# Optimization experiments

Hardware: AMD Instinct MI355X
Metric: run time of the kernel (lower is better)

## Reference

```python
import jax, jax.numpy as jnp
import numpy as np

B, L, D, KSIZE = 16, 2048, 128, 8  # batch, seq_len, d_model (=input=hidden), window size


def setup_inputs() -> dict:
    key = jax.random.key(0)
    ks = jax.random.split(key, 5)
    s = 1.0 / np.sqrt(D)  # PyTorch RNN init range
    return {
        "x": jax.random.normal(ks[0], (B, L, D), jnp.float32),
        "W_ih": jax.random.uniform(ks[1], (3 * D, D), jnp.float32, -s, s),
        "W_hh": jax.random.uniform(ks[2], (3 * D, D), jnp.float32, -s, s),
        "b_ih": jax.random.uniform(ks[3], (3 * D,), jnp.float32, -s, s),
        "b_hh": jax.random.uniform(ks[4], (3 * D,), jnp.float32, -s, s),
    }


def _local_gru(x, W_ih, W_hh, b_ih, b_hh, ksize):
    # x: [B, L, D]. Equivalent to get_K (left zero-pad + sliding windows of
    # length ksize) followed by a GRU over each window, keeping the last
    # hidden state. Instead of materializing [B*L, ksize, D] windows, we scan
    # over the ksize window positions: at step t, every window reads the
    # shifted sequence x_pad[:, t:t+L, :].
    Bb, Ll, Dd = x.shape
    H = W_hh.shape[1]
    pad = jnp.zeros((Bb, ksize - 1, Dd), x.dtype)
    xp = jnp.concatenate([pad, x], axis=1)  # [B, L+k-1, D]
    xs = jnp.stack([xp[:, t:t + Ll, :] for t in range(ksize)], axis=0)  # [k, B, L, D]

    Wir, Wiz, Win = jnp.split(W_ih, 3, axis=0)
    Whr, Whz, Whn = jnp.split(W_hh, 3, axis=0)
    bir, biz, bin_ = jnp.split(b_ih, 3)
    bhr, bhz, bhn = jnp.split(b_hh, 3)

    def step(h, xt):  # h, xt: [B, L, H/D]
        r = jax.nn.sigmoid(xt @ Wir.T + bir + h @ Whr.T + bhr)
        z = jax.nn.sigmoid(xt @ Wiz.T + biz + h @ Whz.T + bhz)
        n = jnp.tanh(xt @ Win.T + bin_ + r * (h @ Whn.T + bhn))
        h = (1.0 - z) * n + z * h
        return h, None

    h0 = jnp.zeros((Bb, Ll, H), x.dtype)
    h_last, _ = jax.lax.scan(step, h0, xs)
    return h_last  # [B, L, H]: last hidden state of each length-ksize window


def reference(x, W_ih, W_hh, b_ih, b_hh):
    return _local_gru(x, W_ih, W_hh, b_ih, b_hh, KSIZE)
```

## Files before the change

### kernel.cpp

```cpp
#include <hip/hip_runtime.h>
#include <hip/hip_bf16.h>

#define DEV __device__ __forceinline__

typedef __attribute__((ext_vector_type(8))) short bf16x8;
typedef __attribute__((ext_vector_type(4))) float f32x4;

constexpr int Bq = 16, Lq = 2048, Dq = 128;
constexpr int RZ = 2 * Dq;
constexpr float L2E = 1.4426950408889634f;

DEV float exp2f_hw(float x) { return __builtin_amdgcn_exp2f(x); }

DEV unsigned short f2bf(float f) {
    union { __hip_bfloat16 h; unsigned short u; } v;
    v.h = __float2bfloat16(f);
    return v.u;
}
DEV float bfu_lo(int u) { return __uint_as_float((unsigned)u << 16); }
DEV float bfu_hi(int u) { return __uint_as_float((unsigned)u & 0xffff0000u); }

DEV float sigm2(float y) { return __builtin_amdgcn_rcpf(1.f + exp2f_hw(-y)); }
DEV float tanh2(float y) {
    float e = exp2f_hw(y);
    return fmaf(-2.f, __builtin_amdgcn_rcpf(e + 1.f), 1.f);
}

DEV bf16x8 pack8s(float4 a, float4 b, float s) {
    bf16x8 r;
    r[0] = (short)f2bf(a.x * s); r[1] = (short)f2bf(a.y * s);
    r[2] = (short)f2bf(a.z * s); r[3] = (short)f2bf(a.w * s);
    r[4] = (short)f2bf(b.x * s); r[5] = (short)f2bf(b.y * s);
    r[6] = (short)f2bf(b.z * s); r[7] = (short)f2bf(b.w * s);
    return r;
}
DEV int2 packbf4(float a, float b, float c, float d) {
    int2 r;
    r.x = (int)(((unsigned)f2bf(b) << 16) | (unsigned)f2bf(a));
    r.y = (int)(((unsigned)f2bf(d) << 16) | (unsigned)f2bf(c));
    return r;
}

__global__ __launch_bounds__(512, 2) void k_proj(
    const float* __restrict__ x, const float* __restrict__ W_ih,
    const float* __restrict__ b_ih, const float* __restrict__ b_hh,
    unsigned short* __restrict__ XpT)
{
    __shared__ __attribute__((aligned(16))) unsigned char lds[96 * 64 * 8];

    const int tid = threadIdx.x;
    const int lane = tid & 63, w = tid >> 6;
    const int l15 = lane & 15, l4 = lane >> 4;
    const int r0 = blockIdx.x * 64;

#pragma unroll
    for (int it = 0; it < 4; ++it) {
        int c = it * 512 + tid;
        int byte = c << 4;
        int row = byte >> 9;
        int wb = byte & 511;
        float4 v = *(const float4*)((const char*)(x + (size_t)r0 * Dq) + byte);
        int dst = row * 256 + ((wb >> 1) ^ ((row & 7) << 4));
        *(int2*)(lds + dst) = packbf4(v.x, v.y, v.z, v.w);
    }

    bf16x8 afr[3][4];
#pragma unroll
    for (int mt = 0; mt < 3; ++mt)
#pragma unroll
        for (int kc = 0; kc < 4; ++kc) {
            int row = 48 * w + 16 * mt + l15;
            int k0 = 32 * kc + 8 * l4;
            const float* p = W_ih + row * Dq + k0;
            afr[mt][kc] = pack8s(*(const float4*)p, *(const float4*)(p + 4), 1.f);
        }
    float fs[3], bias[3][4];
#pragma unroll
    for (int mt = 0; mt < 3; ++mt) {
        int rbase = 48 * w + 16 * mt + 4 * l4;
        fs[mt] = (rbase < RZ) ? L2E : 2.f * L2E;
#pragma unroll
        for (int r = 0; r < 4; ++r) {
            int row = rbase + r;
            float bv = b_ih[row] + (row < RZ ? b_hh[row] : 0.f);
            bias[mt][r] = bv * fs[mt];
        }
    }
    __syncthreads();

    f32x4 acc[3][4];
#pragma unroll
    for (int mt = 0; mt < 3; ++mt)
#pragma unroll
        for (int nt = 0; nt < 4; ++nt) {
            acc[mt][nt][0] = 0.f; acc[mt][nt][1] = 0.f;
            acc[mt][nt][2] = 0.f; acc[mt][nt][3] = 0.f;
        }

#pragma unroll
    for (int kc = 0; kc < 4; ++kc) {
        bf16x8 bfr[4];
#pragma unroll
        for (int nt = 0; nt < 4; ++nt) {
            int row = 16 * nt + l15;
            int off = row * 256 + ((64 * kc + 16 * l4) ^ ((row & 7) << 4));
            bfr[nt] = *(const bf16x8*)(lds + off);
        }
#pragma unroll
        for (int nt = 0; nt < 4; ++nt)
#pragma unroll
            for (int mt = 0; mt < 3; ++mt)
                acc[mt][nt] = __builtin_amdgcn_mfma_f32_16x16x32_bf16(
                    afr[mt][kc], bfr[nt], acc[mt][nt], 0, 0, 0);
    }

    __syncthreads();

#pragma unroll
    for (int mt = 0; mt < 3; ++mt)
#pragma unroll
        for (int nt = 0; nt < 4; ++nt) {
            int r = 16 * nt + l15;
            int g4 = 12 * w + 4 * mt + l4;
            int2 pk = packbf4(fmaf(acc[mt][nt][0], fs[mt], bias[mt][0]),
                              fmaf(acc[mt][nt][1], fs[mt], bias[mt][1]),
                              fmaf(acc[mt][nt][2], fs[mt], bias[mt][2]),
                              fmaf(acc[mt][nt][3], fs[mt], bias[mt][3]));
            *(int2*)(lds + (((g4 << 6) + r) << 3)) = pk;
        }
    __syncthreads();

    {
        const int lr0 = r0 & 2047;
        const int bb = r0 >> 11;
#pragma unroll
        for (int it = 0; it < 6; ++it) {
            int idx = it * 512 + tid;
            int g4 = idx >> 5, off = idx & 31;
            size_t d = (((size_t)(bb * 96 + g4) << 11) + lr0) >> 1;
            ((int4*)XpT)[d + off] = ((const int4*)lds)[idx];
        }
    }
}

__global__ __launch_bounds__(512, 2) void k_rnn(
    const int2* __restrict__ Xp2, const float* __restrict__ W_hh,
    const float* __restrict__ b_ih, const float* __restrict__ b_hh,
    float* __restrict__ out)
{
    __shared__ __attribute__((aligned(16))) unsigned char hls[2 * 32 * 256];

    const int tid = threadIdx.x;
    const int lane = tid & 63, w = tid >> 6;
    const int l15 = lane & 15, l4 = lane >> 4;
    const int b = blockIdx.x >> 6;
    const int l0 = (blockIdx.x & 63) << 5;

    bf16x8 afr[3][4];
#pragma unroll
    for (int g = 0; g < 3; ++g) {
        float fg = (g < 2) ? L2E : 2.f * L2E;
#pragma unroll
        for (int kc = 0; kc < 4; ++kc) {
            int row = 128 * g + 16 * w + l15;
            int k0 = 32 * kc + 8 * l4;
            const float* p = W_hh + row * Dq + k0;
            afr[g][kc] = pack8s(*(const float4*)p, *(const float4*)(p + 4), fg);
        }
    }
    const int u0 = 16 * w + 4 * l4;
    const float4 bir = *(const float4*)(b_ih + u0);
    const float4 bhr = *(const float4*)(b_hh + u0);
    const float4 biz = *(const float4*)(b_ih + Dq + u0);
    const float4 bhz = *(const float4*)(b_hh + Dq + u0);
    const float4 bin_ = *(const float4*)(b_ih + RZ + u0);
    const float4 bhn = *(const float4*)(b_hh + RZ + u0);
    f32x4 bhn4;
    bhn4[0] = bhn.x * (2.f * L2E); bhn4[1] = bhn.y * (2.f * L2E);
    bhn4[2] = bhn.z * (2.f * L2E); bhn4[3] = bhn.w * (2.f * L2E);
    const int2 pbr = packbf4((bir.x + bhr.x) * L2E, (bir.y + bhr.y) * L2E,
                             (bir.z + bhr.z) * L2E, (bir.w + bhr.w) * L2E);
    const int2 pbz = packbf4((biz.x + bhz.x) * L2E, (biz.y + bhz.y) * L2E,
                             (biz.z + bhz.z) * L2E, (biz.w + bhz.w) * L2E);
    const int2 pbn = packbf4(bin_.x * (2.f * L2E), bin_.y * (2.f * L2E),
                             bin_.z * (2.f * L2E), bin_.w * (2.f * L2E));

    const size_t rowr = ((size_t)(b * 96) + (u0 >> 2)) << 11;
    const int2* pr = Xp2 + rowr + (l0 + l15 - 7);
    const int2* pz = pr + (size_t)32 * 2048;
    const int2* pn = pr + (size_t)64 * 2048;
    const bool edge = (l0 == 0);

    f32x4 h[2];

#pragma unroll
    for (int nt = 0; nt < 2; ++nt) {
        int2 qr, qz, qn;
        if (!edge) {
            qr = pr[16 * nt]; qz = pz[16 * nt]; qn = pn[16 * nt];
        } else {
            int ln = 16 * nt + l15 - 7;
            int lnc = ln < 0 ? 0 : ln;
            qr = (Xp2 + rowr)[lnc];
            qz = (Xp2 + rowr + (size_t)32 * 2048)[lnc];
            qn = (Xp2 + rowr + (size_t)64 * 2048)[lnc];
            if (ln < 0) { qr = pbr; qz = pbz; qn = pbn; }
        }
        float xr[4] = {bfu_lo(qr.x), bfu_hi(qr.x), bfu_lo(qr.y), bfu_hi(qr.y)};
        float xz[4] = {bfu_lo(qz.x), bfu_hi(qz.x), bfu_lo(qz.y), bfu_hi(qz.y)};
        float xn[4] = {bfu_lo(qn.x), bfu_hi(qn.x), bfu_lo(qn.y), bfu_hi(qn.y)};
#pragma unroll
        for (int r = 0; r < 4; ++r) {
            float rv = sigm2(xr[r]);
            float zv = sigm2(xz[r]);
            float nv = tanh2(fmaf(rv, bhn4[r], xn[r]));
            h[nt][r] = nv - zv * nv;
        }
    }
#pragma unroll
    for (int nt = 0; nt < 2; ++nt) {
        int win = 16 * nt + l15;
        int off = win * 256 + ((2 * u0) ^ ((win & 7) << 4));
        *(int2*)(hls + off) = packbf4(h[nt][0], h[nt][1], h[nt][2], h[nt][3]);
    }
    __syncthreads();

    for (int t = 1; t < 8; ++t) {
        int2 qr_s[2], qz_s[2], qn_s[2];
        if (!edge) {
#pragma unroll
            for (int nt = 0; nt < 2; ++nt) {
                qr_s[nt] = pr[16 * nt + t];
                qz_s[nt] = pz[16 * nt + t];
                qn_s[nt] = pn[16 * nt + t];
            }
        } else {
#pragma unroll
            for (int nt = 0; nt < 2; ++nt) {
                int ln = 16 * nt + l15 + t - 7;
                int lnc = ln < 0 ? 0 : ln;
                qr_s[nt] = (Xp2 + rowr)[lnc];
                qz_s[nt] = (Xp2 + rowr + (size_t)32 * 2048)[lnc];
                qn_s[nt] = (Xp2 + rowr + (size_t)64 * 2048)[lnc];
                if (ln < 0) { qr_s[nt] = pbr; qz_s[nt] = pbz; qn_s[nt] = pbn; }
            }
        }

        const int rdo = ((t - 1) & 1) << 13;
        const int wro = (t & 1) << 13;
        f32x4 ar[2], az[2], an[2];
#pragma unroll
        for (int nt = 0; nt < 2; ++nt) {
            ar[nt][0] = 0.f; ar[nt][1] = 0.f; ar[nt][2] = 0.f; ar[nt][3] = 0.f;
            az[nt] = ar[nt];
            an[nt] = bhn4;
        }
#pragma unroll
        for (int kc = 0; kc < 4; ++kc) {
            bf16x8 bfr[2];
#pragma unroll
            for (int nt = 0; nt < 2; ++nt) {
                int win = 16 * nt + l15;
                int off = rdo + win * 256 + ((64 * kc + 16 * l4) ^ ((win & 7) << 4));
                bfr[nt] = *(const bf16x8*)(hls + off);
            }
#pragma unroll
            for (int nt = 0; nt < 2; ++nt) {
                ar[nt] = __builtin_amdgcn_mfma_f32_16x16x32_bf16(afr[0][kc], bfr[nt], ar[nt], 0, 0, 0);
                az[nt] = __builtin_amdgcn_mfma_f32_16x16x32_bf16(afr[1][kc], bfr[nt], az[nt], 0, 0, 0);
                an[nt] = __builtin_amdgcn_mfma_f32_16x16x32_bf16(afr[2][kc], bfr[nt], an[nt], 0, 0, 0);
            }
        }
#pragma unroll
        for (int nt = 0; nt < 2; ++nt) {
            float xr[4] = {bfu_lo(qr_s[nt].x), bfu_hi(qr_s[nt].x),
                           bfu_lo(qr_s[nt].y), bfu_hi(qr_s[nt].y)};
            float xz[4] = {bfu_lo(qz_s[nt].x), bfu_hi(qz_s[nt].x),
                           bfu_lo(qz_s[nt].y), bfu_hi(qz_s[nt].y)};
            float xn[4] = {bfu_lo(qn_s[nt].x), bfu_hi(qn_s[nt].x),
                           bfu_lo(qn_s[nt].y), bfu_hi(qn_s[nt].y)};
#pragma unroll
            for (int r = 0; r < 4; ++r) {
                float rv = sigm2(ar[nt][r] + xr[r]);
                float zv = sigm2(az[nt][r] + xz[r]);
                float nv = tanh2(fmaf(rv, an[nt][r], xn[r]));
                h[nt][r] = nv + zv * (h[nt][r] - nv);
            }
        }
        if (t < 7) {
#pragma unroll
            for (int nt = 0; nt < 2; ++nt) {
                int win = 16 * nt + l15;
                int off = wro + win * 256 + ((2 * u0) ^ ((win & 7) << 4));
                *(int2*)(hls + off) = packbf4(h[nt][0], h[nt][1], h[nt][2], h[nt][3]);
            }
            __syncthreads();
        }
    }

#pragma unroll
    for (int nt = 0; nt < 2; ++nt) {
        size_t idx = ((size_t)(b * Lq + l0 + 16 * nt + l15)) * Dq + u0;
        *(f32x4*)(out + idx) = h[nt];
    }
}

extern "C" void kernel_launch(void* const* d_in, const int* in_sizes, int n_in,
                              void* d_out, int out_size, void* d_ws, size_t ws_size,
                              hipStream_t stream) {
    const float* x    = (const float*)d_in[0];
    const float* W_ih = (const float*)d_in[1];
    const float* W_hh = (const float*)d_in[2];
    const float* b_ih = (const float*)d_in[3];
    const float* b_hh = (const float*)d_in[4];
    float* out = (float*)d_out;
    unsigned short* XpT = (unsigned short*)d_ws;

    k_proj<<<dim3(512), dim3(512), 0, stream>>>(x, W_ih, b_ih, b_hh, XpT);
    k_rnn<<<dim3(1024), dim3(512), 0, stream>>>((const int2*)XpT, W_hh, b_ih, b_hh, out);
}
```

Measured before the change: 156.6 us.

## Fuse input projection into recurrent kernel via per-block LDS projection tile

Merges the separate input-projection kernel and the recurrent kernel into one launch. Each block loads its 32 windows plus a 7-row halo of x, converts it to bf16 in LDS, and computes the W_ih projection with MFMA into a swizzled LDS tile. The recurrent steps then read projected inputs from LDS instead of from a global bf16 workspace, and the zero-padded left edge is handled by zero-filled x rows. This removes the global write and reread of the projection buffer and one kernel launch. The cost is recomputing halo rows (48 padded rows per 32 outputs) and higher LDS use per block.

Measured after the change: 157.2 us. No clear change (+0.4%).

```diff
diff --git a/kernel.cpp b/kernel.cpp
--- a/kernel.cpp
+++ b/kernel.cpp
@@ -41,114 +41,13 @@
     return r;
 }
 
-__global__ __launch_bounds__(512, 2) void k_proj(
+__global__ __launch_bounds__(512, 2) void k_fused(
     const float* __restrict__ x, const float* __restrict__ W_ih,
-    const float* __restrict__ b_ih, const float* __restrict__ b_hh,
-    unsigned short* __restrict__ XpT)
+    const float* __restrict__ W_hh, const float* __restrict__ b_ih,
+    const float* __restrict__ b_hh, float* __restrict__ out)
 {
-    __shared__ __attribute__((aligned(16))) unsigned char lds[96 * 64 * 8];
-
-    const int tid = threadIdx.x;
-    const int lane = tid & 63, w = tid >> 6;
-    const int l15 = lane & 15, l4 = lane >> 4;
-    const int r0 = blockIdx.x * 64;
-
-#pragma unroll
-    for (int it = 0; it < 4; ++it) {
-        int c = it * 512 + tid;
-        int byte = c << 4;
-        int row = byte >> 9;
-        int wb = byte & 511;
-        float4 v = *(const float4*)((const char*)(x + (size_t)r0 * Dq) + byte);
-        int dst = row * 256 + ((wb >> 1) ^ ((row & 7) << 4));
-        *(int2*)(lds + dst) = packbf4(v.x, v.y, v.z, v.w);
-    }
-
-    bf16x8 afr[3][4];
-#pragma unroll
-    for (int mt = 0; mt < 3; ++mt)
-#pragma unroll
-        for (int kc = 0; kc < 4; ++kc) {
-            int row = 48 * w + 16 * mt + l15;
-            int k0 = 32 * kc + 8 * l4;
-            const float* p = W_ih + row * Dq + k0;
-            afr[mt][kc] = pack8s(*(const float4*)p, *(const float4*)(p + 4), 1.f);
-        }
-    float fs[3], bias[3][4];
-#pragma unroll
-    for (int mt = 0; mt < 3; ++mt) {
-        int rbase = 48 * w + 16 * mt + 4 * l4;
-        fs[mt] = (rbase < RZ) ? L2E : 2.f * L2E;
-#pragma unroll
-        for (int r = 0; r < 4; ++r) {
-            int row = rbase + r;
-            float bv = b_ih[row] + (row < RZ ? b_hh[row] : 0.f);
-            bias[mt][r] = bv * fs[mt];
-        }
-    }
-    __syncthreads();
-
-    f32x4 acc[3][4];
-#pragma unroll
-    for (int mt = 0; mt < 3; ++mt)
-#pragma unroll
-        for (int nt = 0; nt < 4; ++nt) {
-            acc[mt][nt][0] = 0.f; acc[mt][nt][1] = 0.f;
-            acc[mt][nt][2] = 0.f; acc[mt][nt][3] = 0.f;
-        }
-
-#pragma unroll
-    for (int kc = 0; kc < 4; ++kc) {
-        bf16x8 bfr[4];
-#pragma unroll
-        for (int nt = 0; nt < 4; ++nt) {
-            int row = 16 * nt + l15;
-            int off = row * 256 + ((64 * kc + 16 * l4) ^ ((row & 7) << 4));
-            bfr[nt] = *(const bf16x8*)(lds + off);
-        }
-#pragma unroll
-        for (int nt = 0; nt < 4; ++nt)
-#pragma unroll
-            for (int mt = 0; mt < 3; ++mt)
-                acc[mt][nt] = __builtin_amdgcn_mfma_f32_16x16x32_bf16(
-                    afr[mt][kc], bfr[nt], acc[mt][nt], 0, 0, 0);
-    }
-
-    __syncthreads();
-
-#pragma unroll
-    for (int mt = 0; mt < 3; ++mt)
-#pragma unroll
-        for (int nt = 0; nt < 4; ++nt) {
-            int r = 16 * nt + l15;
-            int g4 = 12 * w + 4 * mt + l4;
-            int2 pk = packbf4(fmaf(acc[mt][nt][0], fs[mt], bias[mt][0]),
-                              fmaf(acc[mt][nt][1], fs[mt], bias[mt][1]),
-                              fmaf(acc[mt][nt][2], fs[mt], bias[mt][2]),
-                              fmaf(acc[mt][nt][3], fs[mt], bias[mt][3]));
-            *(int2*)(lds + (((g4 << 6) + r) << 3)) = pk;
-        }
-    __syncthreads();
-
-    {
-        const int lr0 = r0 & 2047;
-        const int bb = r0 >> 11;
-#pragma unroll
-        for (int it = 0; it < 6; ++it) {
-            int idx = it * 512 + tid;
-            int g4 = idx >> 5, off = idx & 31;
-            size_t d = (((size_t)(bb * 96 + g4) << 11) + lr0) >> 1;
-            ((int4*)XpT)[d + off] = ((const int4*)lds)[idx];
-        }
-    }
-}
-
-__global__ __launch_bounds__(512, 2) void k_rnn(
-    const int2* __restrict__ Xp2, const float* __restrict__ W_hh,
-    const float* __restrict__ b_ih, const float* __restrict__ b_hh,
-    float* __restrict__ out)
-{
-    __shared__ __attribute__((aligned(16))) unsigned char hls[2 * 32 * 256];
+    __shared__ __attribute__((aligned(16))) unsigned char xpt[48 * 768];
+    __shared__ __attribute__((aligned(16))) unsigned char buf2[16384];
 
     const int tid = threadIdx.x;
     const int lane = tid & 63, w = tid >> 6;
@@ -156,56 +55,109 @@
     const int b = blockIdx.x >> 6;
     const int l0 = (blockIdx.x & 63) << 5;
 
+    {
+        const float4* xb = (const float4*)(x + (size_t)b * Lq * Dq);
+#pragma unroll
+        for (int it = 0; it < 3; ++it) {
+            int c = it * 512 + tid;
+            int row = c >> 5, col = c & 31;
+            int l = l0 - 7 + row;
+            float4 v = make_float4(0.f, 0.f, 0.f, 0.f);
+            if (row < 39 && l >= 0) v = xb[(size_t)l * 32 + col];
+            int dst = row * 256 + ((col << 3) ^ ((row & 7) << 4));
+            *(int2*)(buf2 + dst) = packbf4(v.x, v.y, v.z, v.w);
+        }
+    }
+
     bf16x8 afr[3][4];
+#pragma unroll
+    for (int mt = 0; mt < 3; ++mt)
+#pragma unroll
+        for (int kc = 0; kc < 4; ++kc) {
+            int row = 48 * w + 16 * mt + l15;
+            const float* p = W_ih + row * Dq + 32 * kc + 8 * l4;
+            afr[mt][kc] = pack8s(*(const float4*)p, *(const float4*)(p + 4), 1.f);
+        }
+    float fs[3];
+    f32x4 bias[3];
+#pragma unroll
+    for (int mt = 0; mt < 3; ++mt) {
+        int rbase = 48 * w + 16 * mt + 4 * l4;
+        fs[mt] = (rbase < RZ) ? L2E : 2.f * L2E;
+#pragma unroll
+        for (int r = 0; r < 4; ++r) {
+            int row = rbase + r;
+            bias[mt][r] = (b_ih[row] + (row < RZ ? b_hh[row] : 0.f)) * fs[mt];
+        }
+    }
+    __syncthreads();
+
+    {
+        f32x4 acc[3][3];
+#pragma unroll
+        for (int mt = 0; mt < 3; ++mt)
+#pragma unroll
+            for (int nt = 0; nt < 3; ++nt) {
+                acc[mt][nt][0] = 0.f; acc[mt][nt][1] = 0.f;
+                acc[mt][nt][2] = 0.f; acc[mt][nt][3] = 0.f;
+            }
+#pragma unroll
+        for (int kc = 0; kc < 4; ++kc) {
+            bf16x8 bfr[3];
+#pragma unroll
+            for (int nt = 0; nt < 3; ++nt) {
+                int row = 16 * nt + l15;
+                int off = row * 256 + ((64 * kc + 16 * l4) ^ ((row & 7) << 4));
+                bfr[nt] = *(const bf16x8*)(buf2 + off);
+            }
+#pragma unroll
+            for (int nt = 0; nt < 3; ++nt)
+#pragma unroll
+                for (int mt = 0; mt < 3; ++mt)
+                    acc[mt][nt] = __builtin_amdgcn_mfma_f32_16x16x32_bf16(
+                        afr[mt][kc], bfr[nt], acc[mt][nt], 0, 0, 0);
+        }
+#pragma unroll
+        for (int mt = 0; mt < 3; ++mt)
+#pragma unroll
+            for (int nt = 0; nt < 3; ++nt) {
+                int lrow = 16 * nt + l15;
+                int g = 48 * w + 16 * mt + 4 * l4;
+                int sw = (lrow & 7) << 3;
+                int2 pk = packbf4(fmaf(acc[mt][nt][0], fs[mt], bias[mt][0]),
+                                  fmaf(acc[mt][nt][1], fs[mt], bias[mt][1]),
+                                  fmaf(acc[mt][nt][2], fs[mt], bias[mt][2]),
+                                  fmaf(acc[mt][nt][3], fs[mt], bias[mt][3]));
+                *(int2*)(xpt + lrow * 768 + ((g ^ sw) << 1)) = pk;
+            }
+    }
+    __syncthreads();
+
 #pragma unroll
     for (int g = 0; g < 3; ++g) {
         float fg = (g < 2) ? L2E : 2.f * L2E;
 #pragma unroll
         for (int kc = 0; kc < 4; ++kc) {
             int row = 128 * g + 16 * w + l15;
-            int k0 = 32 * kc + 8 * l4;
-            const float* p = W_hh + row * Dq + k0;
+            const float* p = W_hh + row * Dq + 32 * kc + 8 * l4;
             afr[g][kc] = pack8s(*(const float4*)p, *(const float4*)(p + 4), fg);
         }
     }
     const int u0 = 16 * w + 4 * l4;
-    const float4 bir = *(const float4*)(b_ih + u0);
-    const float4 bhr = *(const float4*)(b_hh + u0);
-    const float4 biz = *(const float4*)(b_ih + Dq + u0);
-    const float4 bhz = *(const float4*)(b_hh + Dq + u0);
-    const float4 bin_ = *(const float4*)(b_ih + RZ + u0);
-    const float4 bhn = *(const float4*)(b_hh + RZ + u0);
     f32x4 bhn4;
-    bhn4[0] = bhn.x * (2.f * L2E); bhn4[1] = bhn.y * (2.f * L2E);
-    bhn4[2] = bhn.z * (2.f * L2E); bhn4[3] = bhn.w * (2.f * L2E);
-    const int2 pbr = packbf4((bir.x + bhr.x) * L2E, (bir.y + bhr.y) * L2E,
-                             (bir.z + bhr.z) * L2E, (bir.w + bhr.w) * L2E);
-    const int2 pbz = packbf4((biz.x + bhz.x) * L2E, (biz.y + bhz.y) * L2E,
-                             (biz.z + bhz.z) * L2E, (biz.w + bhz.w) * L2E);
-    const int2 pbn = packbf4(bin_.x * (2.f * L2E), bin_.y * (2.f * L2E),
-                             bin_.z * (2.f * L2E), bin_.w * (2.f * L2E));
-
-    const size_t rowr = ((size_t)(b * 96) + (u0 >> 2)) << 11;
-    const int2* pr = Xp2 + rowr + (l0 + l15 - 7);
-    const int2* pz = pr + (size_t)32 * 2048;
-    const int2* pn = pr + (size_t)64 * 2048;
-    const bool edge = (l0 == 0);
+#pragma unroll
+    for (int r = 0; r < 4; ++r) bhn4[r] = b_hh[RZ + u0 + r] * (2.f * L2E);
 
     f32x4 h[2];
 
 #pragma unroll
     for (int nt = 0; nt < 2; ++nt) {
-        int2 qr, qz, qn;
-        if (!edge) {
-            qr = pr[16 * nt]; qz = pz[16 * nt]; qn = pn[16 * nt];
-        } else {
-            int ln = 16 * nt + l15 - 7;
-            int lnc = ln < 0 ? 0 : ln;
-            qr = (Xp2 + rowr)[lnc];
-            qz = (Xp2 + rowr + (size_t)32 * 2048)[lnc];
-            qn = (Xp2 + rowr + (size_t)64 * 2048)[lnc];
-            if (ln < 0) { qr = pbr; qz = pbz; qn = pbn; }
-        }
+        int tr = 16 * nt + l15;
+        int s = (tr & 7) << 3;
+        const unsigned char* rowp = xpt + tr * 768;
+        int2 qr = *(const int2*)(rowp + ((u0 ^ s) << 1));
+        int2 qz = *(const int2*)(rowp + (((Dq + u0) ^ s) << 1));
+        int2 qn = *(const int2*)(rowp + (((RZ + u0) ^ s) << 1));
         float xr[4] = {bfu_lo(qr.x), bfu_hi(qr.x), bfu_lo(qr.y), bfu_hi(qr.y)};
         float xz[4] = {bfu_lo(qz.x), bfu_hi(qz.x), bfu_lo(qz.y), bfu_hi(qz.y)};
         float xn[4] = {bfu_lo(qn.x), bfu_hi(qn.x), bfu_lo(qn.y), bfu_hi(qn.y)};
@@ -221,33 +173,25 @@
     for (int nt = 0; nt < 2; ++nt) {
         int win = 16 * nt + l15;
         int off = win * 256 + ((2 * u0) ^ ((win & 7) << 4));
-        *(int2*)(hls + off) = packbf4(h[nt][0], h[nt][1], h[nt][2], h[nt][3]);
+        *(int2*)(buf2 + off) = packbf4(h[nt][0], h[nt][1], h[nt][2], h[nt][3]);
     }
     __syncthreads();
 
     for (int t = 1; t < 8; ++t) {
-        int2 qr_s[2], qz_s[2], qn_s[2];
-        if (!edge) {
-#pragma unroll
-            for (int nt = 0; nt < 2; ++nt) {
-                qr_s[nt] = pr[16 * nt + t];
-                qz_s[nt] = pz[16 * nt + t];
-                qn_s[nt] = pn[16 * nt + t];
-            }
-        } else {
-#pragma unroll
-            for (int nt = 0; nt < 2; ++nt) {
-                int ln = 16 * nt + l15 + t - 7;
-                int lnc = ln < 0 ? 0 : ln;
-                qr_s[nt] = (Xp2 + rowr)[lnc];
-                qz_s[nt] = (Xp2 + rowr + (size_t)32 * 2048)[lnc];
-                qn_s[nt] = (Xp2 + rowr + (size_t)64 * 2048)[lnc];
-                if (ln < 0) { qr_s[nt] = pbr; qz_s[nt] = pbz; qn_s[nt] = pbn; }
-            }
-        }
-
         const int rdo = ((t - 1) & 1) << 13;
         const int wro = (t & 1) << 13;
+
+        int2 qr_s[2], qz_s[2], qn_s[2];
+#pragma unroll
+        for (int nt = 0; nt < 2; ++nt) {
+            int tr = 16 * nt + l15 + t;
+            int s = (tr & 7) << 3;
+            const unsigned char* rowp = xpt + tr * 768;
+            qr_s[nt] = *(const int2*)(rowp + ((u0 ^ s) << 1));
+            qz_s[nt] = *(const int2*)(rowp + (((Dq + u0) ^ s) << 1));
+            qn_s[nt] = *(const int2*)(rowp + (((RZ + u0) ^ s) << 1));
+        }
+
         f32x4 ar[2], az[2], an[2];
 #pragma unroll
         for (int nt = 0; nt < 2; ++nt) {
@@ -262,7 +206,7 @@
             for (int nt = 0; nt < 2; ++nt) {
                 int win = 16 * nt + l15;
                 int off = rdo + win * 256 + ((64 * kc + 16 * l4) ^ ((win & 7) << 4));
-                bfr[nt] = *(const bf16x8*)(hls + off);
+                bfr[nt] = *(const bf16x8*)(buf2 + off);
             }
 #pragma unroll
             for (int nt = 0; nt < 2; ++nt) {
@@ -292,7 +236,7 @@
             for (int nt = 0; nt < 2; ++nt) {
                 int win = 16 * nt + l15;
                 int off = wro + win * 256 + ((2 * u0) ^ ((win & 7) << 4));
-                *(int2*)(hls + off) = packbf4(h[nt][0], h[nt][1], h[nt][2], h[nt][3]);
+                *(int2*)(buf2 + off) = packbf4(h[nt][0], h[nt][1], h[nt][2], h[nt][3]);
             }
             __syncthreads();
         }
@@ -314,8 +258,6 @@
     const float* b_ih = (const float*)d_in[3];
     const float* b_hh = (const float*)d_in[4];
     float* out = (float*)d_out;
-    unsigned short* XpT = (unsigned short*)d_ws;
-
-    k_proj<<<dim3(512), dim3(512), 0, stream>>>(x, W_ih, b_ih, b_hh, XpT);
-    k_rnn<<<dim3(1024), dim3(512), 0, stream>>>((const int2*)XpT, W_hh, b_ih, b_hh, out);
-}
+
+    k_fused<<<dim3(1024), dim3(512), 0, stream>>>(x, W_ih, W_hh, b_ih, b_hh, out);
+}
```
